# Kernel optimization log

Measured on AMD Instinct MI355X. Metric: run time of the kernel, lower is better.

Reference implementation:

```python
import jax, jax.numpy as jnp
import numpy as np

T, H, WD = 30, 41, 2048            # timesteps, freq rows, time frames
N_SEC, SEC_LEN, IN_SEC = 9, 4, 6   # conv sections, section stride, input section size
KH, KW = 6, 40                     # conv kernel
FM = 50                            # feature maps
THRESH = 23.0                      # fire threshold
POOL = 4                           # pooling kernel/stride
SEC_H = IN_SEC + SEC_LEN - 1       # 9 rows fed to each section conv


def setup_inputs() -> dict:
    key = jax.random.key(0)
    k1, k2 = jax.random.split(key)
    x = jax.random.uniform(k1, (T, 1, H, WD), dtype=jnp.float32)
    W = jax.random.normal(k2, (N_SEC, FM, 1, KH, KW), dtype=jnp.float32)
    return {"x": x, "W": W}


def _conv_section(sec, w):
    # sec: (T,1,SEC_H,WD) treated as batch of T images; w: (FM,1,KH,KW)
    return jax.lax.conv_general_dilated(
        sec, w, window_strides=(1, 1), padding="VALID",
        dimension_numbers=("NCHW", "OIHW", "NCHW"))


def _forward(x, W):
    # slice 9 overlapping frequency sections: rows i*4 .. i*4+9
    secs = jnp.stack([
        jax.lax.dynamic_slice_in_dim(x, i * SEC_LEN, SEC_H, axis=2)
        for i in range(N_SEC)
    ])  # (9, T, 1, 9, WD)
    pots = jax.vmap(_conv_section)(secs, W)          # (9, T, FM, 4, WD-KW+1)
    spks = (pots > THRESH).astype(pots.dtype)        # sf.fire(threshold=23)
    # snn.Pooling((4,4)) == max_pool2d kernel=stride=(4,4)
    pooled = jax.lax.reduce_window(
        spks, -jnp.inf, jax.lax.max,
        (1, 1, 1, POOL, POOL), (1, 1, 1, POOL, POOL), "VALID")  # (9,T,FM,1,Wp)
    # ties broken by potential at first-spike time; winners[0][0] = feature map.
    has = pooled > 0
    any_spk = has.any(axis=1)                        # (9, FM, 1, Wp)
    t_first = jnp.argmax(has, axis=1)                # (9, FM, 1, Wp)
    pot_at = jnp.take_along_axis(pooled, t_first[:, None], axis=1)[:, 0]
    BIG = jnp.float32(T * 1000.0)
    score = jnp.where(any_spk,
                      (T - t_first).astype(pooled.dtype) * BIG + pot_at,
                      -jnp.inf)                      # (9, FM, 1, Wp)
    flat = score.reshape(N_SEC, -1)
    idx = jnp.argmax(flat, axis=1)
    spatial = score.shape[-1] * score.shape[-2]
    feat = idx // spatial                            # winner feature map per section
    feat = jnp.where(jnp.isneginf(flat.max(axis=1)), -1, feat)  # output=-1 if no winner
    return pooled, feat


def reference(x, W):
    return _forward(x, W)
```

## Files before the change

### kernel.cpp

```cpp
#include <hip/hip_runtime.h>

#define T_ 30
#define H_ 41
#define WD_ 2048
#define NSEC 9
#define FM 50
#define WP 502
#define THRESH 23.0f
#define POOLED_SIZE (NSEC * T_ * FM * WP)
#define MARGIN 0.125f
#define NFRAG 18432

typedef _Float16 half8 __attribute__((ext_vector_type(8)));
typedef _Float16 half4v __attribute__((ext_vector_type(4)));
typedef float f32x4 __attribute__((ext_vector_type(4)));

__device__ __forceinline__ unsigned short f16_bits(float f) {
    union { _Float16 h; unsigned short s; } u;
    u.h = (_Float16)f;
    return u.s;
}

__global__ __launch_bounds__(256) void prep_kernel(
    const float* __restrict__ Wg, int* __restrict__ wsi,
    uint4* __restrict__ wfh)
{
    const int gid = blockIdx.x * 256 + threadIdx.x;
    if (gid < NSEC) wsi[gid] = 0x7fffffff;
    if (gid >= NFRAG) return;
    const int blk = gid & 31;
    const int fm  = (gid >> 5) & 63;
    const int sec = gid >> 11;
    const int t0  = blk * 8;
    const bool valid = (t0 < 240) && (fm < FM);
    const float* wp = Wg + ((size_t)sec * FM + (valid ? fm : 0)) * 240 + (valid ? t0 : 0);
    float4 wa = *reinterpret_cast<const float4*>(wp);
    float4 wb = *reinterpret_cast<const float4*>(wp + 4);
    float f[8] = {wa.x, wa.y, wa.z, wa.w, wb.x, wb.y, wb.z, wb.w};
    unsigned hh[4];
#pragma unroll
    for (int i = 0; i < 4; ++i) {
        unsigned h0 = f16_bits(valid ? f[2 * i] : 0.f);
        unsigned h1 = f16_bits(valid ? f[2 * i + 1] : 0.f);
        hh[i] = (h1 << 16) | h0;
    }
    wfh[gid] = *reinterpret_cast<uint4*>(hh);
}

template <bool PRE>
__global__ __launch_bounds__(256) void conv_pool_kernel(
    const float* __restrict__ x, const float* __restrict__ Wg,
    const uint4* __restrict__ wfh,
    float* __restrict__ out, int* __restrict__ keys)
{
    __shared__ __align__(16) unsigned short xh[4][10][192];
    __shared__ int sred[256];

    const int b       = blockIdx.x;
    const int coltile = b & 15;
    const int tt      = (b >> 4) % T_;
    const int sec     = b / 480;
    const int w0      = coltile * 128;
    const int rowbase = 4 * sec;
    const int tid     = threadIdx.x;

    for (int i = tid; i < 440; i += 256) {
        const int row = i / 44;
        const int c4  = i % 44;
        const int grow = (rowbase + row < H_) ? rowbase + row : H_ - 1;
        const int gc   = w0 + 4 * c4;
        float4 v;
        if (gc + 3 < WD_) {
            v = *reinterpret_cast<const float4*>(x + ((size_t)tt * H_ + grow) * WD_ + gc);
        } else {
            v.x = v.y = v.z = v.w = 0.f;
        }
        float f[4] = {v.x, v.y, v.z, v.w};
        unsigned short hq[4];
#pragma unroll
        for (int e = 0; e < 4; ++e) hq[e] = f16_bits(f[e]);
        const int xr = (row & 7) << 3;
#pragma unroll
        for (int S = 0; S < 4; ++S)
#pragma unroll
            for (int e = 0; e < 4; ++e) {
                const int j = 4 * c4 + e - S;
                if (j >= 0 && j < 176) xh[S][row][j ^ xr] = hq[e];
            }
    }
    __syncthreads();

    const int L    = tid & 63;
    const int j_p  = tid >> 6;
    const int q    = L >> 4;
    const int n16  = L & 15;

    int pA[8], pB[8];
#pragma unroll
    for (int kk = 0; kk < 8; ++kk) {
        const int t0 = 32 * kk + 8 * q;
        const int r  = t0 / 40;
        const int c0 = t0 - 40 * r;
        const int row = j_p + r;
        const int xr  = (row & 7) << 3;
        const int s   = c0 + 8 * n16;
        pA[kk] = row * 192 + (s ^ xr);
        pB[kk] = row * 192 + ((s + 8) ^ xr);
    }

    unsigned mask = 0;

#pragma unroll 1
    for (int ft = 0; ft < 4; ++ft) {
        const int fm = ft * 16 + n16;
        half8 wh[8];
        if (PRE) {
            const int fb = (sec * 64 + ft * 16 + n16) * 32 + q;
#pragma unroll
            for (int kk = 0; kk < 8; ++kk) {
                union { uint4 u; half8 h; } c1;
                c1.u = wfh[fb + 4 * kk];
                wh[kk] = c1.h;
            }
        } else {
#pragma unroll
            for (int kk = 0; kk < 8; ++kk) {
                const int t0 = 32 * kk + 8 * q;
                const bool wvalid = (t0 < 240) && (fm < FM);
                const float* wp = Wg + (size_t)sec * FM * 240 +
                                  (size_t)(wvalid ? fm : 0) * 240 + (wvalid ? t0 : 0);
                float4 wa = *reinterpret_cast<const float4*>(wp);
                float4 wb = *reinterpret_cast<const float4*>(wp + 4);
                float f[8] = {wa.x, wa.y, wa.z, wa.w, wb.x, wb.y, wb.z, wb.w};
                union { unsigned u[4]; half8 h; } c1;
#pragma unroll
                for (int i = 0; i < 4; ++i) {
                    unsigned h0 = f16_bits(wvalid ? f[2 * i] : 0.f);
                    unsigned h1 = f16_bits(wvalid ? f[2 * i + 1] : 0.f);
                    c1.u[i] = (h1 << 16) | h0;
                }
                wh[kk] = c1.h;
            }
        }

        f32x4 vmax0 = {-1e30f, -1e30f, -1e30f, -1e30f};
        f32x4 vmax1 = {-1e30f, -1e30f, -1e30f, -1e30f};

#pragma unroll 1
        for (int S = 0; S < 4; ++S) {
            const unsigned short* hb = &xh[S][0][0];

            f32x4 acc0 = {0.f, 0.f, 0.f, 0.f};
            f32x4 acc1 = {0.f, 0.f, 0.f, 0.f};
#pragma unroll
            for (int kk = 0; kk < 8; ++kk) {
                half8 ah0 = *reinterpret_cast<const half8*>(hb + pA[kk]);
                half4v h0 = *reinterpret_cast<const half4v*>(hb + pA[kk] + 4);
                half4v h1 = *reinterpret_cast<const half4v*>(hb + pB[kk]);
                half8 ah1 = __builtin_shufflevector(h0, h1, 0, 1, 2, 3, 4, 5, 6, 7);
                acc0 = __builtin_amdgcn_mfma_f32_16x16x32_f16(ah0, wh[kk], acc0, 0, 0, 0);
                acc1 = __builtin_amdgcn_mfma_f32_16x16x32_f16(ah1, wh[kk], acc1, 0, 0, 0);
            }
#pragma unroll
            for (int reg = 0; reg < 4; ++reg) {
                vmax0[reg] = fmaxf(vmax0[reg], acc0[reg]);
                vmax1[reg] = fmaxf(vmax1[reg], acc1[reg]);
            }
        }

        auto depilogue = [&](const f32x4& vmax, const int grp) {
#pragma unroll
            for (int reg = 0; reg < 4; ++reg) {
                float v = vmax[reg];
                const int m    = q * 4 + reg;
                const int pcgb = w0 + grp * 4 + 8 * m;
                const bool valid = (fm < FM) && (pcgb <= 2007);
                bool spike = valid && (v > THRESH);
                const bool need = valid && (__builtin_fabsf(v - THRESH) < MARGIN);
                unsigned long long bm = __ballot(need);
                while (bm) {
                    const int src = __ffsll((long long)bm) - 1;
                    bm &= bm - 1;
                    const int q_s    = src >> 4;
                    const int fm_s   = ft * 16 + (src & 15);
                    const int pcgb_s = w0 + grp * 4 + 8 * (q_s * 4 + reg);
                    bool any = false;
#pragma unroll 1
                    for (int c = 0; c < 4; ++c) {
                        float part = 0.f;
#pragma unroll
                        for (int k2 = 0; k2 < 4; ++k2) {
                            const int t = L + 64 * k2;
                            if (t < 240) {
                                const int r2 = t / 40, c2 = t - 40 * r2;
                                part = fmaf(
                                    x[((size_t)tt * H_ + rowbase + j_p + r2) * WD_ + pcgb_s + c + c2],
                                    Wg[(size_t)sec * FM * 240 + (size_t)fm_s * 240 + t],
                                    part);
                            }
                        }
#pragma unroll
                        for (int off = 32; off; off >>= 1)
                            part += __shfl_xor(part, off);
                        any |= (part > THRESH);
                    }
                    if (L == src) spike = any;
                }
                if (spike)
                    mask |= 1u << (reg * 8 + ft * 2 + grp);
            }
        };
        depilogue(vmax0, 0);
        depilogue(vmax1, 1);
    }

    unsigned* lmask = reinterpret_cast<unsigned*>(sred);
    lmask[j_p * 64 + L] = mask;
    __syncthreads();

    int mykey = 0x7fffffff;
    for (int e = tid; e < 2048; e += 256) {
        const int fmo = e >> 5, p = e & 31;
        const int m = p >> 1, rg = p & 1, ftc = fmo >> 4, fn = fmo & 15;
        const int lane = (m >> 2) * 16 + fn;
        const int bitpos = (m & 3) * 8 + ftc * 2 + rg;
        const unsigned bits = lmask[0 * 64 + lane] | lmask[1 * 64 + lane] |
                              lmask[2 * 64 + lane] | lmask[3 * 64 + lane];
        const int pg = coltile * 32 + p;
        const int spk = (bits >> bitpos) & 1u;
        if (fmo < FM && pg < WP) {
            out[((size_t)(sec * T_ + tt) * FM + fmo) * WP + pg] = spk ? 1.0f : 0.0f;
            if (spk) mykey = min(mykey, fmo * WP + pg);
        }
    }
    __syncthreads();
    sred[tid] = mykey;
    __syncthreads();
    for (int s = 128; s > 0; s >>= 1) {
        if (tid < s) sred[tid] = min(sred[tid], sred[tid + s]);
        __syncthreads();
    }
    if (tid == 0 && sred[0] != 0x7fffffff)
        atomicMin(&keys[sec], (tt << 15) | sred[0]);
}

__global__ void init_kernel(int* __restrict__ ws)
{
    if (threadIdx.x < NSEC) ws[threadIdx.x] = 0x7fffffff;
}

__global__ void finalize_kernel(const int* __restrict__ ws, float* __restrict__ out)
{
    const int i = threadIdx.x;
    if (i < NSEC) {
        const int key = ws[i];
        float feat;
        if (key == 0x7fffffff) feat = -1.0f;
        else                   feat = (float)((key & 32767) / WP);
        out[POOLED_SIZE + i] = feat;
    }
}

extern "C" void kernel_launch(void* const* d_in, const int* in_sizes, int n_in,
                              void* d_out, int out_size, void* d_ws, size_t ws_size,
                              hipStream_t stream) {
    const float* x  = (const float*)d_in[0];
    const float* Wg = (const float*)d_in[1];
    float* out = (float*)d_out;
    int*   wsi = (int*)d_ws;
    uint4* wfh = (uint4*)((char*)d_ws + 256);

    const bool pre = ws_size >= 256 + (size_t)NFRAG * 16;
    if (pre) {
        prep_kernel<<<dim3(72), dim3(256), 0, stream>>>(Wg, wsi, wfh);
        conv_pool_kernel<true><<<dim3(4320), dim3(256), 0, stream>>>(x, Wg, wfh, out, wsi);
    } else {
        init_kernel<<<dim3(1), dim3(64), 0, stream>>>(wsi);
        conv_pool_kernel<false><<<dim3(4320), dim3(256), 0, stream>>>(x, Wg, wfh, out, wsi);
    }
    finalize_kernel<<<dim3(1), dim3(16), 0, stream>>>(wsi, out);
}
```

Baseline: 202.0 us.

## Defer near-threshold fp32 recomputation to a separate worklist repair kernel

```diff
diff --git a/kernel.cpp b/kernel.cpp
--- a/kernel.cpp
+++ b/kernel.cpp
@@ -10,6 +10,7 @@
 #define POOLED_SIZE (NSEC * T_ * FM * WP)
 #define MARGIN 0.125f
 #define NFRAG 18432
+#define WLCAP 65536
 
 typedef _Float16 half8 __attribute__((ext_vector_type(8)));
 typedef _Float16 half4v __attribute__((ext_vector_type(4)));
@@ -27,6 +28,7 @@
 {
     const int gid = blockIdx.x * 256 + threadIdx.x;
     if (gid < NSEC) wsi[gid] = 0x7fffffff;
+    if (gid == 16) wsi[16] = 0;
     if (gid >= NFRAG) return;
     const int blk = gid & 31;
     const int fm  = (gid >> 5) & 63;
@@ -51,7 +53,8 @@
 __global__ __launch_bounds__(256) void conv_pool_kernel(
     const float* __restrict__ x, const float* __restrict__ Wg,
     const uint4* __restrict__ wfh,
-    float* __restrict__ out, int* __restrict__ keys)
+    float* __restrict__ out, int* __restrict__ keys,
+    unsigned* __restrict__ wl, unsigned* __restrict__ wlcnt, int wlcap)
 {
     __shared__ __align__(16) unsigned short xh[4][10][192];
     __shared__ int sred[256];
@@ -171,40 +174,34 @@
         auto depilogue = [&](const f32x4& vmax, const int grp) {
 #pragma unroll
             for (int reg = 0; reg < 4; ++reg) {
-                float v = vmax[reg];
+                const float v = vmax[reg];
                 const int m    = q * 4 + reg;
                 const int pcgb = w0 + grp * 4 + 8 * m;
                 const bool valid = (fm < FM) && (pcgb <= 2007);
-                bool spike = valid && (v > THRESH);
-                const bool need = valid && (__builtin_fabsf(v - THRESH) < MARGIN);
-                unsigned long long bm = __ballot(need);
-                while (bm) {
-                    const int src = __ffsll((long long)bm) - 1;
-                    bm &= bm - 1;
-                    const int q_s    = src >> 4;
-                    const int fm_s   = ft * 16 + (src & 15);
-                    const int pcgb_s = w0 + grp * 4 + 8 * (q_s * 4 + reg);
-                    bool any = false;
+                const bool need  = valid && (__builtin_fabsf(v - THRESH) < MARGIN);
+                bool spike = valid && (v > THRESH) && !need;
+                if (need) {
+                    const unsigned slot = atomicAdd(wlcnt, 1u);
+                    if (slot < (unsigned)wlcap) {
+                        wl[slot] = ((unsigned)sec << 24) | ((unsigned)tt << 19) |
+                                   ((unsigned)fm << 13) | ((unsigned)j_p << 11) |
+                                   (unsigned)pcgb;
+                    } else {
+                        bool any = false;
 #pragma unroll 1
-                    for (int c = 0; c < 4; ++c) {
-                        float part = 0.f;
-#pragma unroll
-                        for (int k2 = 0; k2 < 4; ++k2) {
-                            const int t = L + 64 * k2;
-                            if (t < 240) {
+                        for (int c = 0; c < 4; ++c) {
+                            float pot = 0.f;
+#pragma unroll 1
+                            for (int t = 0; t < 240; ++t) {
                                 const int r2 = t / 40, c2 = t - 40 * r2;
-                                part = fmaf(
-                                    x[((size_t)tt * H_ + rowbase + j_p + r2) * WD_ + pcgb_s + c + c2],
-                                    Wg[(size_t)sec * FM * 240 + (size_t)fm_s * 240 + t],
-                                    part);
+                                pot = fmaf(
+                                    x[((size_t)tt * H_ + rowbase + j_p + r2) * WD_ + pcgb + c + c2],
+                                    Wg[(size_t)sec * FM * 240 + (size_t)fm * 240 + t], pot);
                             }
+                            any |= (pot > THRESH);
                         }
-#pragma unroll
-                        for (int off = 32; off; off >>= 1)
-                            part += __shfl_xor(part, off);
-                        any |= (part > THRESH);
+                        spike = any;
                     }
-                    if (L == src) spike = any;
                 }
                 if (spike)
                     mask |= 1u << (reg * 8 + ft * 2 + grp);
@@ -244,9 +241,52 @@
         atomicMin(&keys[sec], (tt << 15) | sred[0]);
 }
 
+__global__ __launch_bounds__(64) void repair_kernel(
+    const float* __restrict__ x, const float* __restrict__ Wg,
+    float* __restrict__ out, int* __restrict__ keys,
+    const unsigned* __restrict__ wl, const unsigned* __restrict__ wlcnt)
+{
+    const int L = threadIdx.x;
+    unsigned count = *wlcnt;
+    if (count > (unsigned)WLCAP) count = WLCAP;
+    for (unsigned e = blockIdx.x; e < count; e += gridDim.x) {
+        const unsigned ent = wl[e];
+        const int sec  = (int)(ent >> 24);
+        const int tt   = (int)((ent >> 19) & 31u);
+        const int fm   = (int)((ent >> 13) & 63u);
+        const int jp   = (int)((ent >> 11) & 3u);
+        const int pcgb = (int)(ent & 2047u);
+        bool any = false;
+#pragma unroll
+        for (int c = 0; c < 4; ++c) {
+            float part = 0.f;
+#pragma unroll
+            for (int k2 = 0; k2 < 4; ++k2) {
+                const int t = L + 64 * k2;
+                if (t < 240) {
+                    const int r2 = t / 40, c2 = t - 40 * r2;
+                    part = fmaf(
+                        x[((size_t)tt * H_ + 4 * sec + jp + r2) * WD_ + pcgb + c + c2],
+                        Wg[(size_t)sec * FM * 240 + (size_t)fm * 240 + t], part);
+                }
+            }
+#pragma unroll
+            for (int off = 32; off; off >>= 1)
+                part += __shfl_xor(part, off);
+            any |= (part > THRESH);
+        }
+        if (L == 0 && any) {
+            const int pg = pcgb >> 2;
+            out[((size_t)(sec * T_ + tt) * FM + fm) * WP + pg] = 1.0f;
+            atomicMin(&keys[sec], (tt << 15) | (fm * WP + pg));
+        }
+    }
+}
+
 __global__ void init_kernel(int* __restrict__ ws)
 {
     if (threadIdx.x < NSEC) ws[threadIdx.x] = 0x7fffffff;
+    if (threadIdx.x == 16) ws[16] = 0;
 }
 
 __global__ void finalize_kernel(const int* __restrict__ ws, float* __restrict__ out)
@@ -269,14 +309,19 @@
     float* out = (float*)d_out;
     int*   wsi = (int*)d_ws;
     uint4* wfh = (uint4*)((char*)d_ws + 256);
-
-    const bool pre = ws_size >= 256 + (size_t)NFRAG * 16;
+    unsigned* wl    = (unsigned*)((char*)d_ws + 256 + (size_t)NFRAG * 16);
+    unsigned* wlcnt = (unsigned*)&wsi[16];
+
+    const bool pre = ws_size >= 256 + (size_t)NFRAG * 16 + (size_t)WLCAP * 4;
     if (pre) {
         prep_kernel<<<dim3(72), dim3(256), 0, stream>>>(Wg, wsi, wfh);
-        conv_pool_kernel<true><<<dim3(4320), dim3(256), 0, stream>>>(x, Wg, wfh, out, wsi);
+        conv_pool_kernel<true><<<dim3(4320), dim3(256), 0, stream>>>(
+            x, Wg, wfh, out, wsi, wl, wlcnt, WLCAP);
+        repair_kernel<<<dim3(1024), dim3(64), 0, stream>>>(x, Wg, out, wsi, wl, wlcnt);
     } else {
         init_kernel<<<dim3(1), dim3(64), 0, stream>>>(wsi);
-        conv_pool_kernel<false><<<dim3(4320), dim3(256), 0, stream>>>(x, Wg, wfh, out, wsi);
+        conv_pool_kernel<false><<<dim3(4320), dim3(256), 0, stream>>>(
+            x, Wg, wfh, out, wsi, (unsigned*)d_ws, wlcnt, 0);
     }
     finalize_kernel<<<dim3(1), dim3(16), 0, stream>>>(wsi, out);
 }
```

Result: slower. 490.2 us (+142.7%).
